# Optimization experiments

Hardware: AMD Instinct MI355X
Metric: run time of the kernel (lower is better)

The kernel has to match this reference:

```python
import jax, jax.numpy as jnp
import numpy as np

T = 8192        # tokens (batch*seq after _flatten_tokens)
HID = 4096      # hidden_size
Q_SIZE = 4096   # num_heads(32) * head_size(128)
KV_SIZE = 1024  # num_kv_heads(8) * head_size(128)
S = 8           # max_loras (slots)
R = 16          # max_lora_rank


def setup_inputs() -> dict:
    key = jax.random.key(0)
    ks = jax.random.split(key, 8)
    x = jax.random.normal(ks[0], (T, HID), dtype=jnp.float32)
    W = jax.random.normal(ks[1], (Q_SIZE + 2 * KV_SIZE, HID), dtype=jnp.float32) * 0.02
    lora_A = jax.random.normal(ks[2], (S, 3, R, HID), dtype=jnp.float32) * 0.02
    lora_B_q = jax.random.normal(ks[3], (S, Q_SIZE, R), dtype=jnp.float32) * 0.02
    lora_B_k = jax.random.normal(ks[4], (S, KV_SIZE, R), dtype=jnp.float32) * 0.02
    lora_B_v = jax.random.normal(ks[5], (S, KV_SIZE, R), dtype=jnp.float32) * 0.02
    # per-slot scaling = alpha / effective_rank (nonzero -> slot active)
    scaling = jax.random.uniform(ks[6], (S,), minval=0.5, maxval=2.0, dtype=jnp.float32)
    token_to_slot = jax.random.randint(ks[7], (T,), 0, S, dtype=jnp.int32)
    return {"x": x, "W": W, "lora_A": lora_A, "lora_B_q": lora_B_q,
            "lora_B_k": lora_B_k, "lora_B_v": lora_B_v, "scaling": scaling,
            "token_to_slot": token_to_slot}


def reference(x, W, lora_A, lora_B_q, lora_B_k, lora_B_v, scaling, token_to_slot):
    # Base fused QKV projection: y = x @ W^T  -> [T, q_size + 2*kv_size]
    y = x @ W.T

    # Token -> slot dispatch as a one-hot mask (slot < 0 would mean no LoRA; all zero row)
    oneh = (token_to_slot[:, None] == jnp.arange(S)[None, :]).astype(x.dtype)  # [T, S]

    # LoRA down-projection for every (token, slot, target): a[t,s,i,r]
    # [T,S,3,R] is tiny (S*3*R per token)
    a = jnp.einsum('th,sirh->tsir', x, lora_A)
    # route + scale: zero out slots the token is not assigned to, apply per-slot scaling
    a = a * (oneh * scaling[None, :])[:, :, None, None]

    # LoRA up-projections per target; contraction over (slot, rank) performs the
    # grouped gather-GEMM-scatter combine in one dense einsum.
    dq = jnp.einsum('tsr,sdr->td', a[:, :, 0], lora_B_q)  # [T, Q_SIZE]
    dk = jnp.einsum('tsr,sdr->td', a[:, :, 1], lora_B_k)  # [T, KV_SIZE]
    dv = jnp.einsum('tsr,sdr->td', a[:, :, 2], lora_B_v)  # [T, KV_SIZE]

    return y + jnp.concatenate([dq, dk, dv], axis=-1)
```

## Files before the change

kernel.cpp:

```cpp
#include <hip/hip_runtime.h>
#include <stdint.h>

#define T_TOK 8192
#define HID   4096
#define NOUT  6144
#define S_SLOTS 8
#define TPAD_MAX 9216

typedef __attribute__((ext_vector_type(8))) short bf16x8;
typedef __attribute__((ext_vector_type(4))) float f32x4;

__device__ __forceinline__ unsigned short f2bf(float f) {
  union { float f; unsigned u; } v; v.f = f;
  unsigned r = v.u + 0x7FFFu + ((v.u >> 16) & 1u);
  return (unsigned short)(r >> 16);
}

__device__ __forceinline__ f32x4 mfma32(bf16x8 a, bf16x8 b, f32x4 c) {
  return __builtin_amdgcn_mfma_f32_16x16x32_bf16(a, b, c, 0, 0, 0);
}

__device__ __forceinline__ void glds16(const void* g, void* l) {
  __builtin_amdgcn_global_load_lds(
      (const __attribute__((address_space(1))) unsigned int*)g,
      (__attribute__((address_space(3))) unsigned int*)l, 16, 0, 0);
}

__global__ void k_sort(const int* __restrict__ t2s, int* __restrict__ perm,
                       int* __restrict__ slotarr, int* __restrict__ meta) {
  __shared__ int cnt[8], cur[8], padoff[9];
  int tid = threadIdx.x;
  if (tid < 8) cnt[tid] = 0;
  __syncthreads();
  for (int t = tid; t < T_TOK; t += 256) atomicAdd(&cnt[t2s[t]], 1);
  __syncthreads();
  if (tid == 0) {
    int o = 0;
    for (int s = 0; s < 8; ++s) { padoff[s] = o; o += ((cnt[s] + 127) >> 7) << 7; }
    padoff[8] = o;
    meta[0] = o;
  }
  __syncthreads();
  if (tid < 8) cur[tid] = padoff[tid];
  int Tpad = padoff[8];
  for (int p = tid; p < TPAD_MAX; p += 256) {
    int s = 0;
    if (p < Tpad) { while (s < 7 && p >= padoff[s + 1]) ++s; }
    perm[p] = -1;
    slotarr[p] = s;
  }
  __syncthreads();
  for (int t = tid; t < T_TOK; t += 256) {
    int s = t2s[t];
    int pos = atomicAdd(&cur[s], 1);
    perm[pos] = t;
  }
}

__global__ void k_convert(const float* __restrict__ src, unsigned short* __restrict__ dst, int n8) {
  int i = blockIdx.x * blockDim.x + threadIdx.x;
  int stride = gridDim.x * blockDim.x;
  for (; i < n8; i += stride) {
    const f32x4* s = (const f32x4*)src + (size_t)i * 2;
    f32x4 a = s[0], b = s[1];
    bf16x8 o;
    o[0]=(short)f2bf(a[0]); o[1]=(short)f2bf(a[1]); o[2]=(short)f2bf(a[2]); o[3]=(short)f2bf(a[3]);
    o[4]=(short)f2bf(b[0]); o[5]=(short)f2bf(b[1]); o[6]=(short)f2bf(b[2]); o[7]=(short)f2bf(b[3]);
    *((bf16x8*)dst + i) = o;
  }
}

__global__ void k_convert_x(const float* __restrict__ x, const int* __restrict__ perm,
                            const int* __restrict__ meta, unsigned short* __restrict__ xb) {
  int p = blockIdx.x;
  int Tpad = meta[0];
  int t = (p < Tpad) ? perm[p] : -1;
  bf16x8* drow = (bf16x8*)(xb + (size_t)p * HID);
  int tid = threadIdx.x;
  if (t >= 0) {
    const f32x4* srow = (const f32x4*)(x + (size_t)t * HID);
    for (int j = tid; j < HID / 8; j += 256) {
      f32x4 a = srow[j * 2], b = srow[j * 2 + 1];
      bf16x8 o;
      o[0]=(short)f2bf(a[0]); o[1]=(short)f2bf(a[1]); o[2]=(short)f2bf(a[2]); o[3]=(short)f2bf(a[3]);
      o[4]=(short)f2bf(b[0]); o[5]=(short)f2bf(b[1]); o[6]=(short)f2bf(b[2]); o[7]=(short)f2bf(b[3]);
      drow[j] = o;
    }
  } else {
    bf16x8 z = {0,0,0,0,0,0,0,0};
    for (int j = tid; j < HID / 8; j += 256) drow[j] = z;
  }
}

__global__ void k_convert_B(const float* __restrict__ Bq, const float* __restrict__ Bk,
                            const float* __restrict__ Bv, unsigned short* __restrict__ Bb) {
  int i = blockIdx.x * blockDim.x + threadIdx.x;
  int stride = gridDim.x * blockDim.x;
  const int total = S_SLOTS * NOUT * 16;
  for (; i < total; i += stride) {
    int s = i / (NOUT * 16);
    int rem = i - s * (NOUT * 16);
    int col = rem >> 4, r = rem & 15;
    float v;
    if (col < 4096)      v = Bq[((size_t)s * 4096 + col) * 16 + r];
    else if (col < 5120) v = Bk[((size_t)s * 1024 + (col - 4096)) * 16 + r];
    else                 v = Bv[((size_t)s * 1024 + (col - 5120)) * 16 + r];
    Bb[i] = f2bf(v);
  }
}

__global__ __launch_bounds__(256) void k_loraA(
    const unsigned short* __restrict__ xb, const unsigned short* __restrict__ Ab,
    const float* __restrict__ scaling, const int* __restrict__ slotarr,
    const int* __restrict__ meta, unsigned short* __restrict__ abf) {
  int p0 = blockIdx.x * 32;
  int Tpad = meta[0];
  if (p0 >= Tpad) return;
  __shared__ float red[3][64 * 24];
  int tid = threadIdx.x, lane = tid & 63, wid = tid >> 6;
  int s = slotarr[p0];
  const unsigned short* A_s = Ab + (size_t)s * 48 * HID;
  int r = lane & 15, g = lane >> 4;
  f32x4 acc[2][3] = {};
  int kbase = wid * (HID / 4);
  for (int k = kbase; k < kbase + HID / 4; k += 32) {
    const unsigned short* xk = xb + (size_t)p0 * HID + k + g * 8;
    bf16x8 a0 = *(const bf16x8*)(xk + (size_t)r * HID);
    bf16x8 a1 = *(const bf16x8*)(xk + (size_t)(r + 16) * HID);
    const unsigned short* ak = A_s + k + g * 8;
    bf16x8 b0 = *(const bf16x8*)(ak + (size_t)r * HID);
    bf16x8 b1 = *(const bf16x8*)(ak + (size_t)(r + 16) * HID);
    bf16x8 b2 = *(const bf16x8*)(ak + (size_t)(r + 32) * HID);
    acc[0][0] = mfma32(a0, b0, acc[0][0]);
    acc[0][1] = mfma32(a0, b1, acc[0][1]);
    acc[0][2] = mfma32(a0, b2, acc[0][2]);
    acc[1][0] = mfma32(a1, b0, acc[1][0]);
    acc[1][1] = mfma32(a1, b1, acc[1][1]);
    acc[1][2] = mfma32(a1, b2, acc[1][2]);
  }
  if (wid > 0) {
    float* dst = &red[wid - 1][lane * 24];
    for (int m = 0; m < 2; ++m)
      for (int n = 0; n < 3; ++n)
        for (int reg = 0; reg < 4; ++reg) dst[(m * 3 + n) * 4 + reg] = acc[m][n][reg];
  }
  __syncthreads();
  if (wid == 0) {
    float sc = scaling[s];
    for (int m = 0; m < 2; ++m)
      for (int n = 0; n < 3; ++n)
        for (int reg = 0; reg < 4; ++reg) {
          int idx = (m * 3 + n) * 4 + reg;
          float v = acc[m][n][reg] + red[0][lane * 24 + idx] + red[1][lane * 24 + idx] +
                    red[2][lane * 24 + idx];
          int row = p0 + m * 16 + g * 4 + reg;
          abf[(size_t)row * 48 + n * 16 + r] = f2bf(v * sc);
        }
  }
}

__global__ __launch_bounds__(256, 2) void k_gemm(
    const unsigned short* __restrict__ xb, const unsigned short* __restrict__ Wb,
    const unsigned short* __restrict__ abf, const unsigned short* __restrict__ Bb,
    const int* __restrict__ perm, const int* __restrict__ slotarr,
    const int* __restrict__ meta, float* __restrict__ out) {
  __shared__ __align__(16) unsigned short As[128 * 64];
  __shared__ __align__(16) unsigned short Bs[128 * 64];
  __shared__ __align__(16) unsigned short As2[128 * 16];
  __shared__ __align__(16) unsigned short Bs2[128 * 16];

  const int Tpad = meta[0];
  const int nblocks = (Tpad >> 7) * 48;
  int bid = (int)blockIdx.x;
  int swz = (bid & 7) * 432 + (bid >> 3);
  if (swz >= nblocks) return;
  const int bm = swz / 48, bn = swz % 48;

  const int tid = threadIdx.x, lane = tid & 63;
  const int wm = tid >> 7, wn = (tid >> 6) & 1;
  const size_t rowA0 = (size_t)bm << 7;
  const size_t rowB0 = (size_t)bn << 7;
  const int s_tile = slotarr[rowA0];
  const int tgt = (bn >= 40) ? 2 : (bn >= 32) ? 1 : 0;

  {
    int i = tid, row = i >> 1, half = i & 1;
    const unsigned short* ga = abf + (rowA0 + row) * 48 + tgt * 16 + half * 8;
    glds16(ga, (char*)As2 + ((i & ~63) << 4));
    const unsigned short* gb = Bb + ((size_t)s_tile * NOUT + ((size_t)bn << 7) + row) * 16 + half * 8;
    glds16(gb, (char*)Bs2 + ((i & ~63) << 4));
  }

  f32x4 acc[4][4] = {};

  for (int k0 = 0; k0 < HID; k0 += 64) {
    __syncthreads();
    #pragma unroll
    for (int it = 0; it < 4; ++it) {
      int i = it * 256 + tid;
      int row = i >> 3;
      int ksrc = ((i & 7) ^ (row & 7)) << 3;
      glds16(xb + (rowA0 + row) * (size_t)HID + k0 + ksrc, (char*)As + ((i & ~63) << 4));
      glds16(Wb + (rowB0 + row) * (size_t)HID + k0 + ksrc, (char*)Bs + ((i & ~63) << 4));
    }
    __syncthreads();
    #pragma unroll
    for (int c = 0; c < 2; ++c) {
      bf16x8 af[4], bfr[4];
      #pragma unroll
      for (int m = 0; m < 4; ++m) {
        int row = (wm << 6) + (m << 4) + (lane & 15);
        int j = ((c << 2) + (lane >> 4)) ^ (lane & 7);
        af[m] = *(const bf16x8*)((const char*)As + row * 128 + j * 16);
      }
      #pragma unroll
      for (int n = 0; n < 4; ++n) {
        int row = (wn << 6) + (n << 4) + (lane & 15);
        int j = ((c << 2) + (lane >> 4)) ^ (lane & 7);
        bfr[n] = *(const bf16x8*)((const char*)Bs + row * 128 + j * 16);
      }
      #pragma unroll
      for (int m = 0; m < 4; ++m)
        #pragma unroll
        for (int n = 0; n < 4; ++n) acc[m][n] = mfma32(af[m], bfr[n], acc[m][n]);
    }
  }

  {
    bf16x8 a2[4], b2[4];
    bf16x8 z = {0,0,0,0,0,0,0,0};
    #pragma unroll
    for (int m = 0; m < 4; ++m) {
      a2[m] = z; b2[m] = z;
      if (lane < 32) {
        int rowa = (wm << 6) + (m << 4) + (lane & 15);
        a2[m] = *(const bf16x8*)((const char*)As2 + rowa * 32 + (lane >> 4) * 16);
        int rowb = (wn << 6) + (m << 4) + (lane & 15);
        b2[m] = *(const bf16x8*)((const char*)Bs2 + rowb * 32 + (lane >> 4) * 16);
      }
    }
    #pragma unroll
    for (int m = 0; m < 4; ++m)
      #pragma unroll
      for (int n = 0; n < 4; ++n) acc[m][n] = mfma32(a2[m], b2[n], acc[m][n]);
  }

  const int colbase = ((int)bn << 7) + (wn << 6);
  #pragma unroll
  for (int m = 0; m < 4; ++m) {
    #pragma unroll
    for (int reg = 0; reg < 4; ++reg) {
      int p = (int)rowA0 + (wm << 6) + (m << 4) + ((lane >> 4) << 2) + reg;
      int t = perm[p];
      if (t < 0) continue;
      float* orow = out + (size_t)t * NOUT + colbase + (lane & 15);
      #pragma unroll
      for (int n = 0; n < 4; ++n) orow[n << 4] = acc[m][n][reg];
    }
  }
}

extern "C" void kernel_launch(void* const* d_in, const int* in_sizes, int n_in,
                              void* d_out, int out_size, void* d_ws, size_t ws_size,
                              hipStream_t stream) {
  const float* x  = (const float*)d_in[0];
  const float* W  = (const float*)d_in[1];
  const float* lA = (const float*)d_in[2];
  const float* Bq = (const float*)d_in[3];
  const float* Bk = (const float*)d_in[4];
  const float* Bv = (const float*)d_in[5];
  const float* sc = (const float*)d_in[6];
  const int* t2s  = (const int*)d_in[7];
  float* out = (float*)d_out;

  char* ws = (char*)d_ws;
  int* perm    = (int*)(ws + 0);
  int* slotarr = (int*)(ws + 36864);
  int* meta    = (int*)(ws + 73728);
  unsigned short* abf = (unsigned short*)(ws + 73984);
  unsigned short* xb  = (unsigned short*)(ws + 958720);
  unsigned short* Wb  = (unsigned short*)(ws + 76456192);
  unsigned short* Ab  = (unsigned short*)(ws + 126787840);
  unsigned short* Bb  = (unsigned short*)(ws + 129933568);

  hipLaunchKernelGGL(k_sort, dim3(1), dim3(256), 0, stream, t2s, perm, slotarr, meta);
  hipLaunchKernelGGL(k_convert, dim3(2048), dim3(256), 0, stream, W, Wb, NOUT * HID / 8);
  hipLaunchKernelGGL(k_convert, dim3(768), dim3(256), 0, stream, lA, Ab, S_SLOTS * 48 * HID / 8);
  hipLaunchKernelGGL(k_convert_B, dim3(768), dim3(256), 0, stream, Bq, Bk, Bv, Bb);
  hipLaunchKernelGGL(k_convert_x, dim3(TPAD_MAX), dim3(256), 0, stream, x, perm, meta, xb);
  hipLaunchKernelGGL(k_loraA, dim3(288), dim3(256), 0, stream, xb, Ab, sc, slotarr, meta, abf);
  hipLaunchKernelGGL(k_gemm, dim3(3456), dim3(256), 0, stream, xb, Wb, abf, Bb, perm, slotarr, meta, out);
}
```

Before: 983.5 us.

## Rewrite main GEMM with 256x256 tiles and 4-stage async LDS pipeline

The main bf16 GEMM moves from 128x128 tiles with 256 threads and a single-buffered, two-barrier K loop to 256x256 tiles with 512 threads. It uses a 4-deep ring of 32-wide K stages loaded via global_load_lds, with explicit vmcnt waits and one barrier per step, so global loads overlap MFMA work. It also adds XCD-aware band swizzling of workgroups and raises MFMA wave priority. Each 256-row tile can span two slots, so the LoRA-B tile is loaded per 128-row half. The LDS swizzle is dropped, and the larger tiles and register footprint may cause bank conflicts or occupancy limits.

```diff
diff --git a/kernel.cpp b/kernel.cpp
--- a/kernel.cpp
+++ b/kernel.cpp
@@ -6,6 +6,7 @@
 #define NOUT  6144
 #define S_SLOTS 8
 #define TPAD_MAX 9216
+#define NKT 128
 
 typedef __attribute__((ext_vector_type(8))) short bf16x8;
 typedef __attribute__((ext_vector_type(4))) float f32x4;
@@ -159,98 +160,141 @@
   }
 }
 
-__global__ __launch_bounds__(256, 2) void k_gemm(
+__global__ __launch_bounds__(512, 2) void k_gemm(
     const unsigned short* __restrict__ xb, const unsigned short* __restrict__ Wb,
     const unsigned short* __restrict__ abf, const unsigned short* __restrict__ Bb,
     const int* __restrict__ perm, const int* __restrict__ slotarr,
     const int* __restrict__ meta, float* __restrict__ out) {
-  __shared__ __align__(16) unsigned short As[128 * 64];
-  __shared__ __align__(16) unsigned short Bs[128 * 64];
-  __shared__ __align__(16) unsigned short As2[128 * 16];
-  __shared__ __align__(16) unsigned short Bs2[128 * 16];
+  __shared__ __align__(16) unsigned short As[4][256 * 32];
+  __shared__ __align__(16) unsigned short Bs[4][256 * 32];
+  __shared__ __align__(16) unsigned short As2[256 * 16];
+  __shared__ __align__(16) unsigned short Bs2[2][256 * 16];
 
   const int Tpad = meta[0];
-  const int nblocks = (Tpad >> 7) * 48;
-  int bid = (int)blockIdx.x;
-  int swz = (bid & 7) * 432 + (bid >> 3);
-  if (swz >= nblocks) return;
-  const int bm = swz / 48, bn = swz % 48;
-
-  const int tid = threadIdx.x, lane = tid & 63;
-  const int wm = tid >> 7, wn = (tid >> 6) & 1;
-  const size_t rowA0 = (size_t)bm << 7;
-  const size_t rowB0 = (size_t)bn << 7;
-  const int s_tile = slotarr[rowA0];
-  const int tgt = (bn >= 40) ? 2 : (bn >= 32) ? 1 : 0;
+  const int nbm = (Tpad + 255) >> 8;
+  const int nwg = nbm * 24;
+  const int bid = (int)blockIdx.x;
+  if (bid >= nwg) return;
+  const int q = nwg >> 3, r = nwg & 7;
+  const int xcd = bid & 7, pos = bid >> 3;
+  const int swz = (xcd < r ? xcd * (q + 1) : r * (q + 1) + (xcd - r) * q) + pos;
+  const int bw = nbm << 2;
+  const int band = swz / bw, rem = swz - band * bw;
+  const int bm = rem >> 2, bn = (band << 2) + (rem & 3);
+
+  const int tid = threadIdx.x, lane = tid & 63, wid = tid >> 6;
+  const int wm = wid >> 2, wn = wid & 3;
+  const int rowA0 = bm << 8;
+  const int rowB0 = bn << 8;
+  const int tgt = (bn >= 20) ? 2 : (bn >= 16) ? 1 : 0;
+  const int s0 = slotarr[rowA0];
+  const int s1 = slotarr[rowA0 + 128];
+
+  const unsigned short* xg = xb + (size_t)rowA0 * HID;
+  const unsigned short* wg = Wb + (size_t)rowB0 * HID;
 
   {
-    int i = tid, row = i >> 1, half = i & 1;
-    const unsigned short* ga = abf + (rowA0 + row) * 48 + tgt * 16 + half * 8;
-    glds16(ga, (char*)As2 + ((i & ~63) << 4));
-    const unsigned short* gb = Bb + ((size_t)s_tile * NOUT + ((size_t)bn << 7) + row) * 16 + half * 8;
-    glds16(gb, (char*)Bs2 + ((i & ~63) << 4));
-  }
-
-  f32x4 acc[4][4] = {};
-
-  for (int k0 = 0; k0 < HID; k0 += 64) {
-    __syncthreads();
-    #pragma unroll
-    for (int it = 0; it < 4; ++it) {
-      int i = it * 256 + tid;
-      int row = i >> 3;
-      int ksrc = ((i & 7) ^ (row & 7)) << 3;
-      glds16(xb + (rowA0 + row) * (size_t)HID + k0 + ksrc, (char*)As + ((i & ~63) << 4));
-      glds16(Wb + (rowB0 + row) * (size_t)HID + k0 + ksrc, (char*)Bs + ((i & ~63) << 4));
-    }
-    __syncthreads();
-    #pragma unroll
-    for (int c = 0; c < 2; ++c) {
-      bf16x8 af[4], bfr[4];
+    int i = tid;
+    glds16(abf + (size_t)(rowA0 + (i >> 1)) * 48 + tgt * 16 + (i & 1) * 8,
+           (char*)As2 + ((i >> 6) << 10));
+    #pragma unroll
+    for (int j = 0; j < 2; ++j) {
+      int ii = j * 512 + tid;
+      int h = ii >> 9, rr = (ii >> 1) & 255, hf = ii & 1;
+      int sh = h ? s1 : s0;
+      glds16(Bb + ((size_t)sh * NOUT + rowB0 + rr) * 16 + hf * 8,
+             (char*)Bs2 + ((ii >> 6) << 10));
+    }
+  }
+
+  auto stage = [&](int kt) {
+    unsigned short* Ad = As[kt & 3];
+    unsigned short* Bd = Bs[kt & 3];
+    const int k0 = kt << 5;
+    #pragma unroll
+    for (int j = 0; j < 2; ++j) {
+      int i = j * 512 + tid;
+      int row = i >> 2, kc = i & 3;
+      glds16(xg + (size_t)row * HID + k0 + kc * 8, (char*)Ad + ((i >> 6) << 10));
+      glds16(wg + (size_t)row * HID + k0 + kc * 8, (char*)Bd + ((i >> 6) << 10));
+    }
+  };
+
+  f32x4 acc[8][4] = {};
+  const int lr = lane & 15, kg = lane >> 4;
+  const int jb = kg << 4;
+
+  auto compute = [&](int kt) {
+    const char* Ap = (const char*)As[kt & 3];
+    const char* Bp = (const char*)Bs[kt & 3];
+    bf16x8 af[8], bfr[4];
+    #pragma unroll
+    for (int m = 0; m < 8; ++m)
+      af[m] = *(const bf16x8*)(Ap + ((wm << 7) + (m << 4) + lr) * 64 + jb);
+    #pragma unroll
+    for (int n = 0; n < 4; ++n)
+      bfr[n] = *(const bf16x8*)(Bp + ((wn << 6) + (n << 4) + lr) * 64 + jb);
+    __builtin_amdgcn_s_setprio(1);
+    #pragma unroll
+    for (int m = 0; m < 8; ++m)
       #pragma unroll
-      for (int m = 0; m < 4; ++m) {
-        int row = (wm << 6) + (m << 4) + (lane & 15);
-        int j = ((c << 2) + (lane >> 4)) ^ (lane & 7);
-        af[m] = *(const bf16x8*)((const char*)As + row * 128 + j * 16);
+      for (int n = 0; n < 4; ++n) acc[m][n] = mfma32(af[m], bfr[n], acc[m][n]);
+    __builtin_amdgcn_s_setprio(0);
+  };
+
+  stage(0); stage(1); stage(2);
+  asm volatile("s_waitcnt vmcnt(8)" ::: "memory");
+  __builtin_amdgcn_s_barrier();
+  __builtin_amdgcn_sched_barrier(0);
+
+  for (int kt = 0; kt < NKT - 3; ++kt) {
+    stage(kt + 3);
+    compute(kt);
+    asm volatile("s_waitcnt vmcnt(8)" ::: "memory");
+    __builtin_amdgcn_s_barrier();
+    __builtin_amdgcn_sched_barrier(0);
+  }
+  compute(NKT - 3);
+  asm volatile("s_waitcnt vmcnt(4)" ::: "memory");
+  __builtin_amdgcn_s_barrier();
+  __builtin_amdgcn_sched_barrier(0);
+  compute(NKT - 2);
+  asm volatile("s_waitcnt vmcnt(0)" ::: "memory");
+  __builtin_amdgcn_s_barrier();
+  __builtin_amdgcn_sched_barrier(0);
+  compute(NKT - 1);
+
+  {
+    bf16x8 z = {0, 0, 0, 0, 0, 0, 0, 0};
+    bf16x8 a2[8], b2[4];
+    #pragma unroll
+    for (int m = 0; m < 8; ++m) {
+      a2[m] = z;
+      if (lane < 32) {
+        int row = (wm << 7) + (m << 4) + lr;
+        a2[m] = *(const bf16x8*)((const char*)As2 + row * 32 + jb);
       }
-      #pragma unroll
-      for (int n = 0; n < 4; ++n) {
-        int row = (wn << 6) + (n << 4) + (lane & 15);
-        int j = ((c << 2) + (lane >> 4)) ^ (lane & 7);
-        bfr[n] = *(const bf16x8*)((const char*)Bs + row * 128 + j * 16);
+    }
+    #pragma unroll
+    for (int n = 0; n < 4; ++n) {
+      b2[n] = z;
+      if (lane < 32) {
+        int col = (wn << 6) + (n << 4) + lr;
+        b2[n] = *(const bf16x8*)((const char*)Bs2 + wm * 8192 + col * 32 + jb);
       }
-      #pragma unroll
-      for (int m = 0; m < 4; ++m)
-        #pragma unroll
-        for (int n = 0; n < 4; ++n) acc[m][n] = mfma32(af[m], bfr[n], acc[m][n]);
-    }
-  }
-
-  {
-    bf16x8 a2[4], b2[4];
-    bf16x8 z = {0,0,0,0,0,0,0,0};
-    #pragma unroll
-    for (int m = 0; m < 4; ++m) {
-      a2[m] = z; b2[m] = z;
-      if (lane < 32) {
-        int rowa = (wm << 6) + (m << 4) + (lane & 15);
-        a2[m] = *(const bf16x8*)((const char*)As2 + rowa * 32 + (lane >> 4) * 16);
-        int rowb = (wn << 6) + (m << 4) + (lane & 15);
-        b2[m] = *(const bf16x8*)((const char*)Bs2 + rowb * 32 + (lane >> 4) * 16);
-      }
-    }
-    #pragma unroll
-    for (int m = 0; m < 4; ++m)
+    }
+    #pragma unroll
+    for (int m = 0; m < 8; ++m)
       #pragma unroll
       for (int n = 0; n < 4; ++n) acc[m][n] = mfma32(a2[m], b2[n], acc[m][n]);
   }
 
-  const int colbase = ((int)bn << 7) + (wn << 6);
+  const int colbase = (bn << 8) + (wn << 6);
   #pragma unroll
-  for (int m = 0; m < 4; ++m) {
+  for (int m = 0; m < 8; ++m) {
     #pragma unroll
     for (int reg = 0; reg < 4; ++reg) {
-      int p = (int)rowA0 + (wm << 6) + (m << 4) + ((lane >> 4) << 2) + reg;
+      int p = rowA0 + (wm << 7) + (m << 4) + ((lane >> 4) << 2) + reg;
       int t = perm[p];
       if (t < 0) continue;
       float* orow = out + (size_t)t * NOUT + colbase + (lane & 15);
@@ -289,5 +333,5 @@
   hipLaunchKernelGGL(k_convert_B, dim3(768), dim3(256), 0, stream, Bq, Bk, Bv, Bb);
   hipLaunchKernelGGL(k_convert_x, dim3(TPAD_MAX), dim3(256), 0, stream, x, perm, meta, xb);
   hipLaunchKernelGGL(k_loraA, dim3(288), dim3(256), 0, stream, xb, Ab, sc, slotarr, meta, abf);
-  hipLaunchKernelGGL(k_gemm, dim3(3456), dim3(256), 0, stream, xb, Wb, abf, Bb, perm, slotarr, meta, out);
-}
+  hipLaunchKernelGGL(k_gemm, dim3(864), dim3(512), 0, stream, xb, Wb, abf, Bb, perm, slotarr, meta, out);
+}
```

Result: slower. 1.073 ms (+9.1%).
